# Kernel optimization log

Hardware: AMD Instinct MI355X
Metric: run time of the kernel (lower is better)

Reference implementation:

```python
import jax, jax.numpy as jnp
import numpy as np

N, L, H, DH = 4, 1024, 16, 64
D = H * DH  # 1024
DFF = 4 * D
NEG_INF = jnp.float32(-1e30)  # used via actual -inf per torch masked_fill


def layer_norm(x, g, b, eps=1e-5):
    mu = jnp.mean(x, axis=-1, keepdims=True)
    var = jnp.mean(jnp.square(x - mu), axis=-1, keepdims=True)
    return (x - mu) * jax.lax.rsqrt(var + eps) * g + b


def mha(q_in, k_in, Wq, Wk, Wv, mask, padding_mask):
    # q_in: (N,Lq,D), k_in: (N,Lk,D); Linear weights (D,D), out = x @ W.T
    n, Lq, _ = q_in.shape
    Lk = k_in.shape[1]
    q = jnp.einsum('nld,od->nlo', q_in, Wq).reshape(n, Lq, H, DH)
    k = jnp.einsum('nld,od->nlo', k_in, Wk).reshape(n, Lk, H, DH)
    v = jnp.einsum('nld,od->nlo', k_in, Wv).reshape(n, Lk, H, DH)
    # per-sample scaling = sqrt(#non-padded keys)
    scaling = jnp.sqrt(jnp.sum(~padding_mask, axis=-1).astype(q.dtype))  # (N,)
    score = jnp.einsum('nqhd,nkhd->nhqk', q, k) / scaling[:, None, None, None]
    if mask is not None:
        score = jnp.where(mask[None, None, :, :], -jnp.inf, score)
    score = jnp.where(padding_mask[:, None, None, :], -jnp.inf, score)
    p = jax.nn.softmax(score, axis=-1)
    out = jnp.einsum('nhqk,nkhd->nqhd', p, v).reshape(n, Lq, D)
    return out


def setup_inputs() -> dict:
    key = jax.random.key(0)
    ks = jax.random.split(key, 16)
    s = 0.02
    inp = {
        'encoded': jax.random.normal(ks[0], (N, L, D), jnp.float32),
        'Y': jax.random.normal(ks[1], (N, L, D), jnp.float32),
        # causal mask: True above diagonal -> attention set to -inf
        'mask': ~jnp.tril(jnp.ones((L, L), dtype=bool)),
        # suffix padding with varied per-sample lengths (all >= 1)
        'padding_mask': jnp.arange(L)[None, :] >= jnp.array([L, 3 * L // 4, L // 2, 7 * L // 8])[:, None],
        # masked self-attention projections
        'Wq1': jax.random.normal(ks[2], (D, D), jnp.float32) * s,
        'Wk1': jax.random.normal(ks[3], (D, D), jnp.float32) * s,
        'Wv1': jax.random.normal(ks[4], (D, D), jnp.float32) * s,
        'g1': jnp.ones((D,), jnp.float32), 'b1': jnp.zeros((D,), jnp.float32),
        # cross-attention projections
        'Wq2': jax.random.normal(ks[5], (D, D), jnp.float32) * s,
        'Wk2': jax.random.normal(ks[6], (D, D), jnp.float32) * s,
        'Wv2': jax.random.normal(ks[7], (D, D), jnp.float32) * s,
        'g2': jnp.ones((D,), jnp.float32), 'b2': jnp.zeros((D,), jnp.float32),
        # FFN
        'We': jax.random.normal(ks[8], (DFF, D), jnp.float32) * s,
        'be': jnp.zeros((DFF,), jnp.float32),
        'Wc': jax.random.normal(ks[9], (D, DFF), jnp.float32) * s,
        'bc': jnp.zeros((D,), jnp.float32),
        'g3': jnp.ones((D,), jnp.float32), 'b3': jnp.zeros((D,), jnp.float32),
    }
    return inp


def reference(encoded, Y, mask, padding_mask,
              Wq1, Wk1, Wv1, g1, b1,
              Wq2, Wk2, Wv2, g2, b2,
              We, be, Wc, bc, g3, b3):
    # masked self-attention + residual + LN (dropout=0 -> identity)
    res = Y
    a = mha(Y, Y, Wq1, Wk1, Wv1, mask, padding_mask)
    Y = layer_norm(a + res, g1, b1)
    # cross-attention (no causal mask) + residual + LN
    res = Y
    a = mha(Y, encoded, Wq2, Wk2, Wv2, None, padding_mask)
    Y = layer_norm(a + res, g2, b2)
    # FFN + residual + LN
    res = Y
    h = jax.nn.relu(jnp.einsum('nld,fd->nlf', Y, We) + be)
    h = jnp.einsum('nlf,df->nld', h, Wc) + bc
    Y = layer_norm(h + res, g3, b3)
    return Y
```

## Files before the change

kernel.cpp:

```cpp
#include <hip/hip_runtime.h>
#include <stdint.h>

#define NB 4
#define LS 1024
#define HH 16
#define DHD 64
#define DM 1024
#define DF 4096
#define QKS 2048

typedef unsigned short u16;
typedef __attribute__((ext_vector_type(4))) float f32x4;
typedef __attribute__((ext_vector_type(8))) __bf16 bf16x8;
typedef __attribute__((ext_vector_type(8))) unsigned short u16x8;

__device__ __forceinline__ u16 f2bf(float f) {
  union { float f; uint32_t u; } v; v.f = f;
  uint32_t u = v.u;
  return (u16)((u + 0x7fffu + ((u >> 16) & 1u)) >> 16);
}

__device__ __forceinline__ bf16x8 ldb8(const u16* p) {
  u16x8 r = *(const u16x8*)p;
  return __builtin_bit_cast(bf16x8, r);
}

__device__ __forceinline__ void gload_lds16(const u16* g, u16* l) {
  __builtin_amdgcn_global_load_lds((const __attribute__((address_space(1))) void*)g,
                                   (__attribute__((address_space(3))) void*)l,
                                   16, 0, 0);
}

#define WAITV8() asm volatile("s_waitcnt vmcnt(8)" ::: "memory")
#define WAITV0() asm volatile("s_waitcnt vmcnt(0)" ::: "memory")
#define WAITLGKM() asm volatile("s_waitcnt lgkmcnt(0)" ::: "memory")
#define PHASE_BARRIER()                        \
  do {                                         \
    WAITLGKM();                                \
    __builtin_amdgcn_sched_barrier(0);         \
    __builtin_amdgcn_s_barrier();              \
    __builtin_amdgcn_sched_barrier(0);         \
  } while (0)

__global__ void prep_kernel(const uint32_t* __restrict__ pm, int* lens, float* iscl) {
  __shared__ int flagByte;
  __shared__ int red[256];
  const int tid = threadIdx.x, n = blockIdx.x;
  if (tid == 0) flagByte = 0;
  __syncthreads();
  int f = 0;
  for (int w = tid; w < (NB * LS) / 4; w += 256) {
    uint32_t u = pm[w];
    if (u != 0u && u != 1u && u != 0x3f800000u) f = 1;
  }
  if (f) atomicOr(&flagByte, 1);
  __syncthreads();
  int c = 0;
  if (flagByte) {
    const uint8_t* pb = (const uint8_t*)pm;
    for (int l = tid; l < LS; l += 256) c += (pb[n * LS + l] == 0) ? 1 : 0;
  } else {
    for (int l = tid; l < LS; l += 256) c += (pm[n * LS + l] == 0) ? 1 : 0;
  }
  red[tid] = c;
  __syncthreads();
  for (int s = 128; s > 0; s >>= 1) {
    if (tid < s) red[tid] += red[tid + s];
    __syncthreads();
  }
  if (tid == 0) { lens[n] = red[0]; iscl[n] = 1.0f / sqrtf((float)red[0]); }
}

__global__ void cvt_all(const float* s0, u16* d0, const float* s1, u16* d1,
                        const float* s2, u16* d2, const float* s3, u16* d3,
                        const float* s4, u16* d4, const float* s5, u16* d5,
                        const float* s6, u16* d6, const float* s7, u16* d7,
                        const float* s8, u16* d8, const float* s9, u16* d9) {
  const int total = 5767168;
  int i = blockIdx.x * 256 + threadIdx.x;
  for (; i < total; i += gridDim.x * 256) {
    const float* s; u16* d; int j;
    if (i < 1048576)      { s = s0; d = d0; j = i; }
    else if (i < 2097152) { s = s1; d = d1; j = i - 1048576; }
    else if (i < 2359296) { s = s2; d = d2; j = i - 2097152; }
    else if (i < 2621440) { s = s3; d = d3; j = i - 2359296; }
    else if (i < 2883584) { s = s4; d = d4; j = i - 2621440; }
    else if (i < 3145728) { s = s5; d = d5; j = i - 2883584; }
    else if (i < 3407872) { s = s6; d = d6; j = i - 3145728; }
    else if (i < 3670016) { s = s7; d = d7; j = i - 3407872; }
    else if (i < 4718592) { s = s8; d = d8; j = i - 3670016; }
    else                  { s = s9; d = d9; j = i - 4718592; }
    float4 fv = ((const float4*)s)[j];
    ushort4 o;
    o.x = f2bf(fv.x); o.y = f2bf(fv.y); o.z = f2bf(fv.z); o.w = f2bf(fv.w);
    ((ushort4*)d)[j] = o;
  }
}

template <int MODE>
__global__ __launch_bounds__(512, 2) void gemm8(
    const u16* __restrict__ P0, const u16* __restrict__ P1,
    const u16* __restrict__ PW, const float* __restrict__ bias,
    void* __restrict__ O0, void* __restrict__ O1,
    void* __restrict__ O2, void* __restrict__ O3) {
  extern __shared__ u16 lds[];
  constexpr int NT = 16;
  const int bm = blockIdx.x;
  const int tid = threadIdx.x;
  const int wid = tid >> 6, lane = tid & 63;
  const int lrow = lane & 15, lgrp = lane >> 4;
  const int wm = wid >> 2, wn = wid & 3;

  const u16* Asrc; const u16* Bsrc; int lda, ldb;
  if constexpr (MODE == 0) {
    Asrc = P0 + (size_t)bm * 256 * DM; lda = DM;
    Bsrc = PW + (size_t)blockIdx.y * 256 * DM; ldb = DM;
  } else if constexpr (MODE == 1) {
    const int z = blockIdx.z;
    Asrc = P0 + (size_t)bm * 256 * DF + z * 1024; lda = DF;
    Bsrc = PW + (size_t)blockIdx.y * 256 * DF + z * 1024; ldb = DF;
  } else {
    const int bnt = blockIdx.y;
    Asrc = (bnt < 12 ? P0 : P1) + (size_t)bm * 256 * DM; lda = DM;
    const int wrow = (bnt < 12) ? bnt * 256 : 4096 + (bnt - 12) * 256;
    Bsrc = PW + (size_t)wrow * DM; ldb = DM;
  }

  int srow[2], skk[2];
#pragma unroll
  for (int i = 0; i < 2; i++) {
    const int c = (i * 8 + wid) * 64 + lane;
    const int pair = c >> 3;
    const int ue = ((c & 7) * 8) ^ ((pair & 7) << 3);
    srow[i] = pair * 2 + (ue >> 5);
    skk[i] = ue & 31;
  }
  const int dslot0 = wid * 512;
  const int dslot1 = (8 + wid) * 512;

  f32x4 acc[2][4][4] = {};

  auto STAGE_A = [&](int kt, int buf, int kh) {
    const int ks = kt < NT ? kt : NT - 1;
    gload_lds16(Asrc + (size_t)srow[0] * lda + ks * 64 + kh * 32 + skk[0],
                lds + buf * 16384 + kh * 8192 + dslot0);
    gload_lds16(Asrc + (size_t)srow[1] * lda + ks * 64 + kh * 32 + skk[1],
                lds + buf * 16384 + kh * 8192 + dslot1);
  };
  auto STAGE_B = [&](int kt, int buf, int kh) {
    const int ks = kt < NT ? kt : NT - 1;
    gload_lds16(Bsrc + (size_t)srow[0] * ldb + ks * 64 + kh * 32 + skk[0],
                lds + 32768 + buf * 16384 + kh * 8192 + dslot0);
    gload_lds16(Bsrc + (size_t)srow[1] * ldb + ks * 64 + kh * 32 + skk[1],
                lds + 32768 + buf * 16384 + kh * 8192 + dslot1);
  };
  auto LDA = [&](int buf, int kh, int mh, bf16x8* a) {
#pragma unroll
    for (int m = 0; m < 4; m++) {
      const int row = wm * 128 + mh * 64 + m * 16 + lrow;
      const int idx = buf * 16384 + kh * 8192 + (row >> 1) * 64 +
                      ((((row & 1) << 5) + (lgrp << 3)) ^ (((row >> 1) & 7) << 3));
      a[m] = ldb8(lds + idx);
    }
  };
  auto LDB = [&](int buf, int kh, bf16x8* b) {
#pragma unroll
    for (int nn = 0; nn < 4; nn++) {
      const int row = wn * 64 + nn * 16 + lrow;
      const int idx = 32768 + buf * 16384 + kh * 8192 + (row >> 1) * 64 +
                      ((((row & 1) << 5) + (lgrp << 3)) ^ (((row >> 1) & 7) << 3));
      b[nn] = ldb8(lds + idx);
    }
  };
  auto MFMA16 = [&](f32x4 (&a4)[4][4], bf16x8* af, bf16x8* bk) {
    __builtin_amdgcn_s_setprio(1);
#pragma unroll
    for (int m = 0; m < 4; m++)
#pragma unroll
      for (int nn = 0; nn < 4; nn++)
        a4[m][nn] = __builtin_amdgcn_mfma_f32_16x16x32_bf16(af[m], bk[nn], a4[m][nn], 0, 0, 0);
    __builtin_amdgcn_s_setprio(0);
  };

  STAGE_A(0, 0, 0); STAGE_B(0, 0, 0);
  STAGE_A(0, 0, 1); STAGE_B(0, 0, 1);
  STAGE_A(1, 1, 0); STAGE_B(1, 1, 0);
  WAITV8();
  __builtin_amdgcn_s_barrier();
  __builtin_amdgcn_sched_barrier(0);

  for (int t = 0; t < NT; t++) {
    const int b = t & 1;
    bf16x8 af[4], bk[4];
    LDA(b, 0, 0, af); LDB(b, 0, bk);
    STAGE_A(t + 1, b ^ 1, 1);
    PHASE_BARRIER();
    MFMA16(acc[0], af, bk);
    LDA(b, 0, 1, af);
    STAGE_B(t + 1, b ^ 1, 1);
    WAITV8();
    PHASE_BARRIER();
    MFMA16(acc[1], af, bk);
    LDA(b, 1, 0, af); LDB(b, 1, bk);
    STAGE_A(t + 2, b, 0);
    PHASE_BARRIER();
    MFMA16(acc[0], af, bk);
    LDA(b, 1, 1, af);
    STAGE_B(t + 2, b, 0);
    WAITV8();
    PHASE_BARRIER();
    MFMA16(acc[1], af, bk);
  }
  WAITV0();

#pragma unroll
  for (int mh = 0; mh < 2; mh++)
#pragma unroll
    for (int m = 0; m < 4; m++) {
      const int grow0 = bm * 256 + wm * 128 + mh * 64 + m * 16 + lgrp * 4;
#pragma unroll
      for (int nn = 0; nn < 4; nn++) {
        const int col_l = wn * 64 + nn * 16 + lrow;
        f32x4 v = acc[mh][m][nn];
        if constexpr (MODE == 0) {
          const int col = blockIdx.y * 256 + col_l;
          const float bv = bias[col];
#pragma unroll
          for (int r = 0; r < 4; r++) {
            float x = v[r] + bv;
            x = x > 0.0f ? x : 0.0f;
            ((u16*)O0)[(size_t)(grow0 + r) * DF + col] = f2bf(x);
          }
        } else if constexpr (MODE == 1) {
          float* C = (float*)O0 + (size_t)blockIdx.z * ((size_t)NB * LS * DM);
          const int col = blockIdx.y * 256 + col_l;
#pragma unroll
          for (int r = 0; r < 4; r++) C[(size_t)(grow0 + r) * DM + col] = v[r];
        } else {
          const int bnt = blockIdx.y;
          const int nidx = grow0 >> 10, l0 = grow0 & 1023;
          if (bnt < 8) {
            const int col = bnt * 256 + col_l;
#pragma unroll
            for (int r = 0; r < 4; r++)
              ((u16*)O0)[(size_t)(grow0 + r) * QKS + col] = f2bf(v[r]);
          } else if (bnt < 12) {
            const int vc = (bnt - 8) * 256 + col_l;
            ushort4 o;
            o.x = f2bf(v[0]); o.y = f2bf(v[1]); o.z = f2bf(v[2]); o.w = f2bf(v[3]);
            *(ushort4*)((u16*)O1 + (((size_t)(nidx * HH + (vc >> 6)) * DHD + (vc & 63)) << 10) + l0) = o;
          } else {
            const int col = 1024 + (bnt - 12) * 256 + col_l;
#pragma unroll
            for (int r = 0; r < 4; r++)
              ((u16*)O2)[(size_t)(grow0 + r) * QKS + col] = f2bf(v[r]);
          }
        }
      }
    }
}

__global__ __launch_bounds__(256) void gemm_qv(const u16* __restrict__ Ya,
                                               const u16* __restrict__ Ea,
                                               const u16* __restrict__ Wq,
                                               const u16* __restrict__ Wv,
                                               u16* __restrict__ QKb,
                                               u16* __restrict__ VtB) {
  __shared__ u16 Al[128 * 32];
  __shared__ u16 Bl[128 * 32];
  const int tid = threadIdx.x;
  const int bm = blockIdx.x, bnr = blockIdx.y;
  const bool isV = bnr >= 8;
  const int bn = isV ? bnr - 8 : bnr;
  const int wave = tid >> 6, lane = tid & 63;
  const int lrow = lane & 15, lgrp = lane >> 4;
  const int wr = (wave >> 1) * 64, wc = (wave & 1) * 64;
  f32x4 acc[4][4] = {};
  const u16* Ab = (isV ? Ea : Ya) + (size_t)bm * 128 * DM;
  const u16* Bb = (isV ? Wv : Wq) + (size_t)bn * 128 * DM;
  {
    const int c0 = wave, c1 = wave + 4;
    const int r0 = c0 * 16 + (lane >> 2), r1 = c1 * 16 + (lane >> 2);
    const int scc = (lane & 3) * 8;
    const u16* Ag0 = Ab + (size_t)r0 * DM + scc;
    const u16* Ag1 = Ab + (size_t)r1 * DM + scc;
    const u16* Bg0 = Bb + (size_t)r0 * DM + scc;
    const u16* Bg1 = Bb + (size_t)r1 * DM + scc;
    u16* Ad0 = Al + c0 * 512;
    u16* Ad1 = Al + c1 * 512;
    u16* Bd0 = Bl + c0 * 512;
    u16* Bd1 = Bl + c1 * 512;
    for (int kb = 0; kb < DM; kb += 32) {
      gload_lds16(Ag0, Ad0);
      gload_lds16(Ag1, Ad1);
      gload_lds16(Bg0, Bd0);
      gload_lds16(Bg1, Bd1);
      Ag0 += 32; Ag1 += 32; Bg0 += 32; Bg1 += 32;
      __syncthreads();
      bf16x8 af[4], bfr[4];
#pragma unroll
      for (int m = 0; m < 4; m++) af[m] = ldb8(Al + (wr + m * 16 + lrow) * 32 + lgrp * 8);
#pragma unroll
      for (int nn = 0; nn < 4; nn++) bfr[nn] = ldb8(Bl + (wc + nn * 16 + lrow) * 32 + lgrp * 8);
#pragma unroll
      for (int m = 0; m < 4; m++)
#pragma unroll
        for (int nn = 0; nn < 4; nn++)
          acc[m][nn] = __builtin_amdgcn_mfma_f32_16x16x32_bf16(af[m], bfr[nn], acc[m][nn], 0, 0, 0);
      __syncthreads();
    }
  }
#pragma unroll
  for (int m = 0; m < 4; m++) {
    const int row0 = bm * 128 + wr + m * 16 + lgrp * 4;
    const int nidx = row0 >> 10, l0 = row0 & (LS - 1);
#pragma unroll
    for (int nn = 0; nn < 4; nn++) {
      const int col = bn * 128 + wc + nn * 16 + lrow;
      if (!isV) {
#pragma unroll
        for (int r = 0; r < 4; r++)
          QKb[(size_t)(row0 + r) * QKS + col] = f2bf(acc[m][nn][r]);
      } else {
        const int hh = col >> 6, dd = col & 63;
        ushort4 o;
        o.x = f2bf(acc[m][nn][0]); o.y = f2bf(acc[m][nn][1]);
        o.z = f2bf(acc[m][nn][2]); o.w = f2bf(acc[m][nn][3]);
        *(ushort4*)(VtB + (((size_t)(nidx * HH + hh) * DHD + dd) << 10) + l0) = o;
      }
    }
  }
}

template <bool CAUSAL>
__global__ __launch_bounds__(256) void attn_kernel(const u16* __restrict__ QK,
                                                   const u16* __restrict__ Vt,
                                                   float* __restrict__ Out,
                                                   const int* __restrict__ lens,
                                                   const float* __restrict__ iscl) {
  __shared__ u16 Kl[64 * 72];
  __shared__ u16 Vl[64 * 72];
  __shared__ u16 Pl[4][16 * 72];
  const int n = blockIdx.z, h = blockIdx.y, qb = blockIdx.x * 64;
  const int tid = threadIdx.x, wave = tid >> 6, lane = tid & 63;
  const int lrow = lane & 15, lgrp = lane >> 4;
  const int len = lens[n];
  const float isc = iscl[n];
  const int qrow = qb + wave * 16 + lrow;
  const u16* qptr = QK + ((size_t)(n * LS + qrow)) * QKS + h * DHD + lgrp * 8;
  bf16x8 qf0 = ldb8(qptr);
  bf16x8 qf1 = ldb8(qptr + 32);
  f32x4 oacc[4] = {};
  float m_run = -1e30f, l_run = 0.0f;
  const int kend = CAUSAL ? (len < qb + 64 ? len : qb + 64) : len;
  const int srow = tid >> 3, sc = (tid & 7) * 8;
  const u16* kg_base = QK + 1024 + ((size_t)(n * LS)) * QKS + h * DHD + sc;
  const u16* vg_base = Vt + ((size_t)((n * HH + h) * DHD) + srow) * LS + sc;
  u16* pw = Pl[wave];
  for (int kb = 0; kb < kend; kb += 64) {
    __syncthreads();
#pragma unroll
    for (int i = 0; i < 2; i++) {
      const int row = srow + i * 32;
      u16x8 kv = *(const u16x8*)(kg_base + (size_t)(kb + row) * QKS);
      *(u16x8*)(Kl + row * 72 + sc) = kv;
      u16x8 vv = *(const u16x8*)(vg_base + (size_t)(i * 32) * LS + kb);
      *(u16x8*)(Vl + row * 72 + sc) = vv;
    }
    __syncthreads();
    f32x4 s[4];
#pragma unroll
    for (int st = 0; st < 4; st++) {
      const u16* kr = Kl + (st * 16 + lrow) * 72 + lgrp * 8;
      bf16x8 kf0 = ldb8(kr);
      bf16x8 kf1 = ldb8(kr + 32);
      f32x4 z = {};
      z = __builtin_amdgcn_mfma_f32_16x16x32_bf16(kf0, qf0, z, 0, 0, 0);
      s[st] = __builtin_amdgcn_mfma_f32_16x16x32_bf16(kf1, qf1, z, 0, 0, 0);
    }
#pragma unroll
    for (int st = 0; st < 4; st++) {
#pragma unroll
      for (int r = 0; r < 4; r++) {
        const int k = kb + st * 16 + lgrp * 4 + r;
        float v = s[st][r] * isc;
        bool ok = (k < len) && (!CAUSAL || k <= qrow);
        s[st][r] = ok ? v : -1e30f;
      }
    }
    float pmax = s[0][0];
#pragma unroll
    for (int st = 0; st < 4; st++)
#pragma unroll
      for (int r = 0; r < 4; r++) pmax = fmaxf(pmax, s[st][r]);
    pmax = fmaxf(pmax, __shfl_xor(pmax, 16));
    pmax = fmaxf(pmax, __shfl_xor(pmax, 32));
    const bool skip = __all(pmax <= m_run + 8.0f);
    float fac = 1.0f;
    if (!skip) {
      float mn = fmaxf(m_run, pmax);
      fac = __expf(m_run - mn);
      m_run = mn;
    }
    float sm = 0.0f;
#pragma unroll
    for (int st = 0; st < 4; st++)
#pragma unroll
      for (int r = 0; r < 4; r++) {
        float p = __expf(s[st][r] - m_run);
        s[st][r] = p;
        sm += p;
      }
    sm += __shfl_xor(sm, 16);
    sm += __shfl_xor(sm, 32);
    l_run = l_run * fac + sm;
    if (!skip) {
#pragma unroll
      for (int r = 0; r < 4; r++) {
        float fr = __shfl(fac, (lane & 48) | (lgrp * 4 + r));
#pragma unroll
        for (int dt = 0; dt < 4; dt++) oacc[dt][r] *= fr;
      }
    }
#pragma unroll
    for (int st = 0; st < 4; st++) {
      uint32_t w0, w1;
      asm("v_cvt_pk_bf16_f32 %0, %1, %2" : "=v"(w0) : "v"(s[st][0]), "v"(s[st][1]));
      asm("v_cvt_pk_bf16_f32 %0, %1, %2" : "=v"(w1) : "v"(s[st][2]), "v"(s[st][3]));
      uint2 wv; wv.x = w0; wv.y = w1;
      *(uint2*)(pw + lrow * 72 + st * 16 + lgrp * 4) = wv;
    }
#pragma unroll
    for (int ks = 0; ks < 2; ks++) {
      bf16x8 pf = ldb8(pw + lrow * 72 + ks * 32 + lgrp * 8);
#pragma unroll
      for (int dt = 0; dt < 4; dt++) {
        bf16x8 vf = ldb8(Vl + (dt * 16 + lrow) * 72 + ks * 32 + lgrp * 8);
        oacc[dt] = __builtin_amdgcn_mfma_f32_16x16x32_bf16(pf, vf, oacc[dt], 0, 0, 0);
      }
    }
  }
#pragma unroll
  for (int r = 0; r < 4; r++) {
    float lr = __shfl(l_run, (lane & 48) | (lgrp * 4 + r));
    float inv = 1.0f / lr;
    const int row = qb + wave * 16 + lgrp * 4 + r;
    float* op = Out + ((size_t)(n * LS + row)) * DM + h * DHD;
#pragma unroll
    for (int dt = 0; dt < 4; dt++) op[dt * 16 + lrow] = oacc[dt][r] * inv;
  }
}

__global__ __launch_bounds__(256) void ln_kernel(const float* __restrict__ a,
                                                 const float* __restrict__ res,
                                                 const float* __restrict__ g,
                                                 const float* __restrict__ bta,
                                                 float* __restrict__ outf,
                                                 u16* __restrict__ outb) {
  const int row = blockIdx.x, tid = threadIdx.x;
  float4 x = ((const float4*)(a + (size_t)row * DM))[tid];
  float4 rr = ((const float4*)(res + (size_t)row * DM))[tid];
  x.x += rr.x; x.y += rr.y; x.z += rr.z; x.w += rr.w;
  float s = x.x + x.y + x.z + x.w;
  float s2 = x.x * x.x + x.y * x.y + x.z * x.z + x.w * x.w;
#pragma unroll
  for (int m = 1; m < 64; m <<= 1) { s += __shfl_xor(s, m); s2 += __shfl_xor(s2, m); }
  __shared__ float sm[8];
  const int wv = tid >> 6;
  if ((tid & 63) == 0) { sm[wv] = s; sm[4 + wv] = s2; }
  __syncthreads();
  s = sm[0] + sm[1] + sm[2] + sm[3];
  s2 = sm[4] + sm[5] + sm[6] + sm[7];
  const float mean = s * (1.0f / (float)DM);
  const float var = s2 * (1.0f / (float)DM) - mean * mean;
  const float inv = rsqrtf(var + 1e-5f);
  float4 gg = ((const float4*)g)[tid];
  float4 bb = ((const float4*)bta)[tid];
  float4 y;
  y.x = (x.x - mean) * inv * gg.x + bb.x;
  y.y = (x.y - mean) * inv * gg.y + bb.y;
  y.z = (x.z - mean) * inv * gg.z + bb.z;
  y.w = (x.w - mean) * inv * gg.w + bb.w;
  ((float4*)(outf + (size_t)row * DM))[tid] = y;
  if (outb) {
    ushort4 o;
    o.x = f2bf(y.x); o.y = f2bf(y.y); o.z = f2bf(y.z); o.w = f2bf(y.w);
    ((ushort4*)(outb + (size_t)row * DM))[tid] = o;
  }
}

__global__ __launch_bounds__(256) void ln_final(const float* __restrict__ part,
                                                const float* __restrict__ bias,
                                                const float* __restrict__ res,
                                                const float* __restrict__ g,
                                                const float* __restrict__ bta,
                                                float* __restrict__ outf) {
  const int row = blockIdx.x, tid = threadIdx.x;
  const size_t PS = (size_t)NB * LS * DM;
  float4 x = ((const float4*)(part + (size_t)row * DM))[tid];
  float4 p1 = ((const float4*)(part + PS + (size_t)row * DM))[tid];
  float4 p2 = ((const float4*)(part + 2 * PS + (size_t)row * DM))[tid];
  float4 p3 = ((const float4*)(part + 3 * PS + (size_t)row * DM))[tid];
  float4 bb4 = ((const float4*)bias)[tid];
  float4 rr = ((const float4*)(res + (size_t)row * DM))[tid];
  x.x += p1.x + p2.x + p3.x + bb4.x + rr.x;
  x.y += p1.y + p2.y + p3.y + bb4.y + rr.y;
  x.z += p1.z + p2.z + p3.z + bb4.z + rr.z;
  x.w += p1.w + p2.w + p3.w + bb4.w + rr.w;
  float s = x.x + x.y + x.z + x.w;
  float s2 = x.x * x.x + x.y * x.y + x.z * x.z + x.w * x.w;
#pragma unroll
  for (int m = 1; m < 64; m <<= 1) { s += __shfl_xor(s, m); s2 += __shfl_xor(s2, m); }
  __shared__ float sm[8];
  const int wv = tid >> 6;
  if ((tid & 63) == 0) { sm[wv] = s; sm[4 + wv] = s2; }
  __syncthreads();
  s = sm[0] + sm[1] + sm[2] + sm[3];
  s2 = sm[4] + sm[5] + sm[6] + sm[7];
  const float mean = s * (1.0f / (float)DM);
  const float var = s2 * (1.0f / (float)DM) - mean * mean;
  const float inv = rsqrtf(var + 1e-5f);
  float4 gg = ((const float4*)g)[tid];
  float4 bb = ((const float4*)bta)[tid];
  float4 y;
  y.x = (x.x - mean) * inv * gg.x + bb.x;
  y.y = (x.y - mean) * inv * gg.y + bb.y;
  y.z = (x.z - mean) * inv * gg.z + bb.z;
  y.w = (x.w - mean) * inv * gg.w + bb.w;
  ((float4*)(outf + (size_t)row * DM))[tid] = y;
}

extern "C" void kernel_launch(void* const* d_in, const int* in_sizes, int n_in,
                              void* d_out, int out_size, void* d_ws, size_t ws_size,
                              hipStream_t stream) {
  const float* enc = (const float*)d_in[0];
  const float* Yin = (const float*)d_in[1];
  const uint32_t* pmask = (const uint32_t*)d_in[3];
  const float* Wq1 = (const float*)d_in[4];
  const float* Wk1 = (const float*)d_in[5];
  const float* Wv1 = (const float*)d_in[6];
  const float* g1 = (const float*)d_in[7];
  const float* b1 = (const float*)d_in[8];
  const float* Wq2 = (const float*)d_in[9];
  const float* Wk2 = (const float*)d_in[10];
  const float* Wv2 = (const float*)d_in[11];
  const float* g2 = (const float*)d_in[12];
  const float* b2 = (const float*)d_in[13];
  const float* We = (const float*)d_in[14];
  const float* be = (const float*)d_in[15];
  const float* Wc = (const float*)d_in[16];
  const float* bc = (const float*)d_in[17];
  const float* g3 = (const float*)d_in[18];
  const float* b3 = (const float*)d_in[19];

  const size_t ACT = (size_t)NB * LS * DM;
  const size_t WSZ = (size_t)DM * DM;
  const size_t WFF = (size_t)DF * DM;
  const size_t HID = (size_t)NB * LS * DF;

  char* ws = (char*)d_ws;
  size_t off = 0;
  auto alloc = [&](size_t bytes) -> void* {
    void* p = ws + off;
    off += (bytes + 255) & ~(size_t)255;
    return p;
  };
  int* lens = (int*)alloc(64);
  float* iscl = (float*)alloc(64);
  u16* Ybf = (u16*)alloc(ACT * 2);
  u16* Ebf = (u16*)alloc(ACT * 2);
  u16* W6 = (u16*)alloc(WSZ * 6 * 2);
  u16* Web = (u16*)alloc(WFF * 2);
  u16* Wcb = (u16*)alloc(WFF * 2);
  size_t region0 = off;
  u16* QKa = (u16*)alloc((size_t)NB * LS * QKS * 2);
  u16* VtA = (u16*)alloc(ACT * 2);
  u16* QKb = (u16*)alloc((size_t)NB * LS * QKS * 2);
  u16* VtB = (u16*)alloc(ACT * 2);
  float* aout = (float*)alloc(ACT * 4);
  float* y2 = (float*)alloc(ACT * 4);
  float* part = (float*)(ws + region0);
  float* y3 = (float*)alloc(ACT * 4);
  u16* Hb = (u16*)alloc(HID * 2);

  prep_kernel<<<NB, 256, 0, stream>>>(pmask, lens, iscl);
  cvt_all<<<2048, 256, 0, stream>>>(Yin, Ybf, enc, Ebf,
                                    Wq1, W6 + 0 * WSZ, Wk1, W6 + 1 * WSZ,
                                    Wv1, W6 + 2 * WSZ, Wq2, W6 + 3 * WSZ,
                                    Wk2, W6 + 4 * WSZ, Wv2, W6 + 5 * WSZ,
                                    We, Web, Wc, Wcb);

  dim3 blk(256);
  gemm8<2><<<dim3(16, 16), 512, 131072, stream>>>(Ybf, Ebf, W6, nullptr,
                                                  QKa, VtA, QKb, VtB);
  attn_kernel<true><<<dim3(16, 16, 4), blk, 0, stream>>>(QKa, VtA, aout, lens, iscl);
  ln_kernel<<<NB * LS, 256, 0, stream>>>(aout, Yin, g1, b1, y2, Ybf);
  gemm_qv<<<dim3(32, 16), blk, 0, stream>>>(Ybf, Ebf, W6 + 3 * WSZ, W6 + 5 * WSZ,
                                            QKb, VtB);
  attn_kernel<false><<<dim3(16, 16, 4), blk, 0, stream>>>(QKb, VtB, aout, lens, iscl);
  ln_kernel<<<NB * LS, 256, 0, stream>>>(aout, y2, g2, b2, y3, Ebf);
  gemm8<0><<<dim3(16, 16), 512, 131072, stream>>>(Ebf, nullptr, Web, be,
                                                  Hb, nullptr, nullptr, nullptr);
  gemm8<1><<<dim3(16, 4, 4), 512, 131072, stream>>>(Hb, nullptr, Wcb, nullptr,
                                                    part, nullptr, nullptr, nullptr);
  ln_final<<<NB * LS, 256, 0, stream>>>(part, bc, y3, g3, b3, (float*)d_out);
}
```

Before: 297.8 us.

## Fold softmax scale into Q projection, prefetch K/V, skip unneeded masking

The per-sample 1/sqrt(len) scale and log2(e) are now multiplied into Q when the projection GEMMs store it, so the attention kernels use exp2 directly and no longer scale each score. The attention loop loads the next K/V tile into registers before computing on the current one, overlapping global loads with MFMA work. Masking runs only on tiles that cross the padding or causal boundary. The trade-offs are extra registers for the prefetch, Q being rounded to bf16 after scaling, and a rescale threshold adjusted to base 2.

```diff
diff --git a/kernel.cpp b/kernel.cpp
--- a/kernel.cpp
+++ b/kernel.cpp
@@ -8,6 +8,7 @@
 #define DM 1024
 #define DF 4096
 #define QKS 2048
+#define LOG2E 1.4426950408889634f
 
 typedef unsigned short u16;
 typedef __attribute__((ext_vector_type(4))) float f32x4;
@@ -102,7 +103,8 @@
     const u16* __restrict__ P0, const u16* __restrict__ P1,
     const u16* __restrict__ PW, const float* __restrict__ bias,
     void* __restrict__ O0, void* __restrict__ O1,
-    void* __restrict__ O2, void* __restrict__ O3) {
+    void* __restrict__ O2, void* __restrict__ O3,
+    const float* __restrict__ iscl) {
   extern __shared__ u16 lds[];
   constexpr int NT = 16;
   const int bm = blockIdx.x;
@@ -240,10 +242,11 @@
           const int bnt = blockIdx.y;
           const int nidx = grow0 >> 10, l0 = grow0 & 1023;
           if (bnt < 8) {
+            const float qs = (bnt < 4) ? iscl[nidx] * LOG2E : 1.0f;
             const int col = bnt * 256 + col_l;
 #pragma unroll
             for (int r = 0; r < 4; r++)
-              ((u16*)O0)[(size_t)(grow0 + r) * QKS + col] = f2bf(v[r]);
+              ((u16*)O0)[(size_t)(grow0 + r) * QKS + col] = f2bf(v[r] * qs);
           } else if (bnt < 12) {
             const int vc = (bnt - 8) * 256 + col_l;
             ushort4 o;
@@ -265,7 +268,8 @@
                                                const u16* __restrict__ Wq,
                                                const u16* __restrict__ Wv,
                                                u16* __restrict__ QKb,
-                                               u16* __restrict__ VtB) {
+                                               u16* __restrict__ VtB,
+                                               const float* __restrict__ iscl) {
   __shared__ u16 Al[128 * 32];
   __shared__ u16 Bl[128 * 32];
   const int tid = threadIdx.x;
@@ -318,9 +322,10 @@
     for (int nn = 0; nn < 4; nn++) {
       const int col = bn * 128 + wc + nn * 16 + lrow;
       if (!isV) {
+        const float qs = iscl[nidx] * LOG2E;
 #pragma unroll
         for (int r = 0; r < 4; r++)
-          QKb[(size_t)(row0 + r) * QKS + col] = f2bf(acc[m][nn][r]);
+          QKb[(size_t)(row0 + r) * QKS + col] = f2bf(acc[m][nn][r] * qs);
       } else {
         const int hh = col >> 6, dd = col & 63;
         ushort4 o;
@@ -336,8 +341,7 @@
 __global__ __launch_bounds__(256) void attn_kernel(const u16* __restrict__ QK,
                                                    const u16* __restrict__ Vt,
                                                    float* __restrict__ Out,
-                                                   const int* __restrict__ lens,
-                                                   const float* __restrict__ iscl) {
+                                                   const int* __restrict__ lens) {
   __shared__ u16 Kl[64 * 72];
   __shared__ u16 Vl[64 * 72];
   __shared__ u16 Pl[4][16 * 72];
@@ -345,7 +349,6 @@
   const int tid = threadIdx.x, wave = tid >> 6, lane = tid & 63;
   const int lrow = lane & 15, lgrp = lane >> 4;
   const int len = lens[n];
-  const float isc = iscl[n];
   const int qrow = qb + wave * 16 + lrow;
   const u16* qptr = QK + ((size_t)(n * LS + qrow)) * QKS + h * DHD + lgrp * 8;
   bf16x8 qf0 = ldb8(qptr);
@@ -357,17 +360,24 @@
   const u16* kg_base = QK + 1024 + ((size_t)(n * LS)) * QKS + h * DHD + sc;
   const u16* vg_base = Vt + ((size_t)((n * HH + h) * DHD) + srow) * LS + sc;
   u16* pw = Pl[wave];
+  u16x8 kreg[2], vreg[2];
+  auto LOADKV = [&](int kb) {
+#pragma unroll
+    for (int i = 0; i < 2; i++) {
+      kreg[i] = *(const u16x8*)(kg_base + (size_t)(kb + srow + i * 32) * QKS);
+      vreg[i] = *(const u16x8*)(vg_base + (size_t)(i * 32) * LS + kb);
+    }
+  };
+  LOADKV(0);
   for (int kb = 0; kb < kend; kb += 64) {
     __syncthreads();
 #pragma unroll
     for (int i = 0; i < 2; i++) {
-      const int row = srow + i * 32;
-      u16x8 kv = *(const u16x8*)(kg_base + (size_t)(kb + row) * QKS);
-      *(u16x8*)(Kl + row * 72 + sc) = kv;
-      u16x8 vv = *(const u16x8*)(vg_base + (size_t)(i * 32) * LS + kb);
-      *(u16x8*)(Vl + row * 72 + sc) = vv;
+      *(u16x8*)(Kl + (srow + i * 32) * 72 + sc) = kreg[i];
+      *(u16x8*)(Vl + (srow + i * 32) * 72 + sc) = vreg[i];
     }
     __syncthreads();
+    if (kb + 64 < kend) LOADKV(kb + 64);
     f32x4 s[4];
 #pragma unroll
     for (int st = 0; st < 4; st++) {
@@ -378,15 +388,16 @@
       z = __builtin_amdgcn_mfma_f32_16x16x32_bf16(kf0, qf0, z, 0, 0, 0);
       s[st] = __builtin_amdgcn_mfma_f32_16x16x32_bf16(kf1, qf1, z, 0, 0, 0);
     }
-#pragma unroll
-    for (int st = 0; st < 4; st++) {
-#pragma unroll
-      for (int r = 0; r < 4; r++) {
-        const int k = kb + st * 16 + lgrp * 4 + r;
-        float v = s[st][r] * isc;
-        bool ok = (k < len) && (!CAUSAL || k <= qrow);
-        s[st][r] = ok ? v : -1e30f;
-      }
+    const bool needMask = (kb + 64 > len) || (CAUSAL && (kb + 64 > qb + wave * 16));
+    if (needMask) {
+#pragma unroll
+      for (int st = 0; st < 4; st++)
+#pragma unroll
+        for (int r = 0; r < 4; r++) {
+          const int k = kb + st * 16 + lgrp * 4 + r;
+          bool ok = (k < len) && (!CAUSAL || k <= qrow);
+          s[st][r] = ok ? s[st][r] : -1e30f;
+        }
     }
     float pmax = s[0][0];
 #pragma unroll
@@ -395,11 +406,11 @@
       for (int r = 0; r < 4; r++) pmax = fmaxf(pmax, s[st][r]);
     pmax = fmaxf(pmax, __shfl_xor(pmax, 16));
     pmax = fmaxf(pmax, __shfl_xor(pmax, 32));
-    const bool skip = __all(pmax <= m_run + 8.0f);
+    const bool skip = __all(pmax <= m_run + 11.541560327f);
     float fac = 1.0f;
     if (!skip) {
       float mn = fmaxf(m_run, pmax);
-      fac = __expf(m_run - mn);
+      fac = exp2f(m_run - mn);
       m_run = mn;
     }
     float sm = 0.0f;
@@ -407,7 +418,7 @@
     for (int st = 0; st < 4; st++)
 #pragma unroll
       for (int r = 0; r < 4; r++) {
-        float p = __expf(s[st][r] - m_run);
+        float p = exp2f(s[st][r] - m_run);
         s[st][r] = p;
         sm += p;
       }
@@ -592,16 +603,16 @@
 
   dim3 blk(256);
   gemm8<2><<<dim3(16, 16), 512, 131072, stream>>>(Ybf, Ebf, W6, nullptr,
-                                                  QKa, VtA, QKb, VtB);
-  attn_kernel<true><<<dim3(16, 16, 4), blk, 0, stream>>>(QKa, VtA, aout, lens, iscl);
+                                                  QKa, VtA, QKb, VtB, iscl);
+  attn_kernel<true><<<dim3(16, 16, 4), blk, 0, stream>>>(QKa, VtA, aout, lens);
   ln_kernel<<<NB * LS, 256, 0, stream>>>(aout, Yin, g1, b1, y2, Ybf);
   gemm_qv<<<dim3(32, 16), blk, 0, stream>>>(Ybf, Ebf, W6 + 3 * WSZ, W6 + 5 * WSZ,
-                                            QKb, VtB);
-  attn_kernel<false><<<dim3(16, 16, 4), blk, 0, stream>>>(QKb, VtB, aout, lens, iscl);
+                                            QKb, VtB, iscl);
+  attn_kernel<false><<<dim3(16, 16, 4), blk, 0, stream>>>(QKb, VtB, aout, lens);
   ln_kernel<<<NB * LS, 256, 0, stream>>>(aout, y2, g2, b2, y3, Ebf);
   gemm8<0><<<dim3(16, 16), 512, 131072, stream>>>(Ebf, nullptr, Web, be,
-                                                  Hb, nullptr, nullptr, nullptr);
+                                                  Hb, nullptr, nullptr, nullptr, nullptr);
   gemm8<1><<<dim3(16, 4, 4), 512, 131072, stream>>>(Hb, nullptr, Wcb, nullptr,
-                                                    part, nullptr, nullptr, nullptr);
+                                                    part, nullptr, nullptr, nullptr, nullptr);
   ln_final<<<NB * LS, 256, 0, stream>>>(part, bc, y3, g3, b3, (float*)d_out);
 }
```

Measured after the change: 287.5 us. -3.5%, faster.
